# Kernel optimization log

Measured on AMD Instinct MI355X. Metric: run time of the kernel, lower is better.

Reference implementation:

```python
import jax, jax.numpy as jnp
import numpy as np

N_HEADS = 16
N_KV_HEADS = 4
HEAD_DIM = 128


def apply_rope(x, cos, sin):
    # x: [b, h, s, head_dim]; cos/sin: [1, 1, s, head_dim//2]
    d = x.shape[-1] // 2
    x1, x2 = x[..., :d], x[..., d:]
    return jnp.concatenate([x1 * cos - x2 * sin, x1 * sin + x2 * cos], axis=-1)


def setup_inputs() -> dict:
    key = jax.random.key(0)
    ks = jax.random.split(key, 9)
    b, s, dim = 2, 2048, 2048
    inp = {
        "x": jax.random.normal(ks[0], (b, s, dim), jnp.float32),
        "cos": jax.random.normal(ks[1], (1, 1, s, HEAD_DIM // 2), jnp.float32),
        "sin": jax.random.normal(ks[2], (1, 1, s, HEAD_DIM // 2), jnp.float32),
        "Wq": jax.random.normal(ks[3], (dim, N_HEADS * HEAD_DIM), jnp.float32) * 0.02,
        "bq": jax.random.normal(ks[4], (N_HEADS * HEAD_DIM,), jnp.float32) * 0.02,
        "Wkv": jax.random.normal(ks[5], (dim, 2 * N_KV_HEADS * HEAD_DIM), jnp.float32) * 0.02,
        "bkv": jax.random.normal(ks[6], (2 * N_KV_HEADS * HEAD_DIM,), jnp.float32) * 0.02,
        "Wo": jax.random.normal(ks[7], (N_HEADS * HEAD_DIM, dim), jnp.float32) * 0.02,
        "bo": jax.random.normal(ks[8], (dim,), jnp.float32) * 0.02,
        "causal": 1,
    }
    return inp


def reference(x, cos, sin, Wq, bq, Wkv, bkv, Wo, bo, causal):
    b, s, dim = x.shape
    scale = 1.0 / np.sqrt(HEAD_DIM)
    # QKV projections (torch Linear with weight stored transposed here)
    q = (x @ Wq + bq).reshape(b, s, N_HEADS, HEAD_DIM).transpose(0, 2, 1, 3)
    kv = x @ Wkv + bkv  # [b, s, 2*n_kv*hd]
    k, v = jnp.split(kv, 2, axis=-1)
    k = k.reshape(b, s, N_KV_HEADS, HEAD_DIM).transpose(0, 2, 1, 3)
    v = v.reshape(b, s, N_KV_HEADS, HEAD_DIM).transpose(0, 2, 1, 3)
    q = apply_rope(q, cos, sin)
    k = apply_rope(k, cos, sin)
    # GQA: repeat kv heads
    rep = N_HEADS // N_KV_HEADS
    k = jnp.repeat(k, rep, axis=1)
    v = jnp.repeat(v, rep, axis=1)
    logits = jnp.einsum("bhqd,bhkd->bhqk", q, k) * scale
    if causal:
        mask = jnp.tril(jnp.ones((s, s), dtype=bool))
        logits = jnp.where(mask[None, None], logits, jnp.finfo(logits.dtype).min)
    scores = jax.nn.softmax(logits, axis=-1)
    vo = jnp.einsum("bhqk,bhkd->bhqd", scores, v)
    vo = vo.transpose(0, 2, 1, 3).reshape(b, s, N_HEADS * HEAD_DIM)
    out = vo @ Wo + bo
    return out
```

## Files before the change

kernel.cpp:

```cpp
#include <hip/hip_runtime.h>
#include <hip/hip_bf16.h>

typedef __bf16 bf16x8 __attribute__((ext_vector_type(8)));
typedef float  f32x4  __attribute__((ext_vector_type(4)));
typedef unsigned int u32;

#define GLD_LDS16(gp, lp) __builtin_amdgcn_global_load_lds( \
    (const __attribute__((address_space(1))) u32*)(gp), \
    (__attribute__((address_space(3))) u32*)(lp), 16, 0, 0)

template<int CTRL>
__device__ __forceinline__ float dpp_rot(float x) {
    int y = __builtin_amdgcn_update_dpp(__float_as_int(x), __float_as_int(x),
                                        CTRL, 0xF, 0xF, false);
    return __int_as_float(y);
}
__device__ __forceinline__ float rowmax16(float x) {
    x = fmaxf(x, dpp_rot<0x121>(x));
    x = fmaxf(x, dpp_rot<0x122>(x));
    x = fmaxf(x, dpp_rot<0x124>(x));
    x = fmaxf(x, dpp_rot<0x128>(x));
    return x;
}
__device__ __forceinline__ float rowsum16(float x) {
    x += dpp_rot<0x121>(x);
    x += dpp_rot<0x122>(x);
    x += dpp_rot<0x124>(x);
    x += dpp_rot<0x128>(x);
    return x;
}


__global__ __launch_bounds__(256) void f32_to_bf16_kernel(
    const float* __restrict__ in, __bf16* __restrict__ out, size_t n) {
    size_t i = ((size_t)blockIdx.x * 256 + threadIdx.x) * 8;
    if (i >= n) return;
    float4 a = *(const float4*)(in + i);
    float4 b = *(const float4*)(in + i + 4);
    bf16x8 v;
    v[0] = (__bf16)a.x; v[1] = (__bf16)a.y; v[2] = (__bf16)a.z; v[3] = (__bf16)a.w;
    v[4] = (__bf16)b.x; v[5] = (__bf16)b.y; v[6] = (__bf16)b.z; v[7] = (__bf16)b.w;
    *(bf16x8*)(out + i) = v;
}

__global__ __launch_bounds__(256) void transpose_to_bf16_kernel(
    const float* __restrict__ W, __bf16* __restrict__ Wt, int K, int N) {
    __shared__ float tile[32][33];
    int n0 = blockIdx.x * 32, k0 = blockIdx.y * 32;
    int tx = threadIdx.x, ty = threadIdx.y;
    #pragma unroll
    for (int i = 0; i < 32; i += 8)
        tile[ty + i][tx] = W[(size_t)(k0 + ty + i) * N + n0 + tx];
    __syncthreads();
    #pragma unroll
    for (int i = 0; i < 32; i += 8)
        Wt[(size_t)(n0 + ty + i) * K + k0 + tx] = (__bf16)tile[tx][ty + i];
}

__global__ __launch_bounds__(256) void transpose_v_kernel(
    const __bf16* __restrict__ kv, __bf16* __restrict__ vtg, int S) {
    __shared__ __bf16 tile[32][33];
    int s0 = blockIdx.x * 32, d0 = blockIdx.y * 32, z = blockIdx.z;
    int b = z >> 2, kvh = z & 3;
    int tx = threadIdx.x, ty = threadIdx.y;
    #pragma unroll
    for (int i = 0; i < 32; i += 8)
        tile[ty + i][tx] = kv[((size_t)b * S + s0 + ty + i) * 1024 + 512 + kvh * 128 + d0 + tx];
    __syncthreads();
    #pragma unroll
    for (int i = 0; i < 32; i += 8)
        vtg[((size_t)z * 128 + d0 + ty + i) * S + s0 + tx] = tile[tx][ty + i];
}

#define BM 128
#define BN 128
#define BK 32

template <typename OutT>
__global__ __launch_bounds__(256) void gemm_bt_bias_kernel(
    const __bf16* __restrict__ A, const __bf16* __restrict__ Bt,
    const float* __restrict__ bias, OutT* __restrict__ C,
    int M, int N, int K) {
    __shared__ __bf16 As[BM][BK];
    __shared__ __bf16 Bs[BN][BK];
    int tid  = threadIdx.x;
    int bm   = blockIdx.x;
    int bn   = blockIdx.y;
    int wave = tid >> 6;
    int lane = tid & 63;
    int wm   = (wave >> 1) * 64;
    int wn   = (wave & 1) * 64;
    int quad = lane >> 4;
    int l16  = lane & 15;
    int srow = wave * 16 + (lane >> 2);
    int scol = (lane & 3) * 8;

    f32x4 acc[4][4];
    f32x4 zero = {0.f, 0.f, 0.f, 0.f};
    #pragma unroll
    for (int i = 0; i < 4; ++i)
        #pragma unroll
        for (int j = 0; j < 4; ++j) acc[i][j] = zero;

    const __bf16* Abase = A  + (size_t)(bm * BM) * K;
    const __bf16* Bbase = Bt + (size_t)(bn * BN) * K;

    for (int k0 = 0; k0 < K; k0 += BK) {
        if (k0) __syncthreads();
        #pragma unroll
        for (int it = 0; it < 2; ++it) {
            int r = it * 64 + srow;
            GLD_LDS16(Abase + (size_t)r * K + k0 + scol, &As[it * 64 + wave * 16][0]);
            GLD_LDS16(Bbase + (size_t)r * K + k0 + scol, &Bs[it * 64 + wave * 16][0]);
        }
        __syncthreads();

        bf16x8 a_frag[4], b_frag[4];
        #pragma unroll
        for (int i = 0; i < 4; ++i)
            a_frag[i] = *(bf16x8*)(&As[wm + i * 16 + l16][quad * 8]);
        #pragma unroll
        for (int j = 0; j < 4; ++j)
            b_frag[j] = *(bf16x8*)(&Bs[wn + j * 16 + l16][quad * 8]);
        #pragma unroll
        for (int i = 0; i < 4; ++i)
            #pragma unroll
            for (int j = 0; j < 4; ++j)
                acc[i][j] = __builtin_amdgcn_mfma_f32_16x16x32_bf16(
                    a_frag[i], b_frag[j], acc[i][j], 0, 0, 0);
    }

    #pragma unroll
    for (int i = 0; i < 4; ++i) {
        int row = bm * BM + wm + i * 16 + quad * 4;
        #pragma unroll
        for (int j = 0; j < 4; ++j) {
            int col  = bn * BN + wn + j * 16 + l16;
            float bv = bias[col];
            #pragma unroll
            for (int r = 0; r < 4; ++r)
                C[(size_t)(row + r) * N + col] = (OutT)(acc[i][j][r] + bv);
        }
    }
}

__global__ __launch_bounds__(256) void rope_kernel(
    __bf16* __restrict__ buf, const float* __restrict__ cosp,
    const float* __restrict__ sinp, int heads, int rowstride, int S, int total) {
    int idx = blockIdx.x * 256 + threadIdx.x;
    if (idx >= total) return;
    int d  = idx & 63;
    int t2 = idx >> 6;
    int h  = t2 % heads;
    int r  = t2 / heads;
    int s  = r & (S - 1);
    size_t base = (size_t)r * rowstride + h * 128;
    float x1 = (float)buf[base + d];
    float x2 = (float)buf[base + d + 64];
    float c  = cosp[s * 64 + d];
    float sn = sinp[s * 64 + d];
    buf[base + d]      = (__bf16)(x1 * c - x2 * sn);
    buf[base + d + 64] = (__bf16)(x1 * sn + x2 * c);
}

#define FB_K   64
#define PS_STR 72

__global__ __launch_bounds__(256, 2) void flash_mfma_kernel(
    const __bf16* __restrict__ q,
    const __bf16* __restrict__ kv,
    const __bf16* __restrict__ vtg,
    __bf16* __restrict__ vo,
    const int* __restrict__ causal_p, int S) {
    __shared__ __bf16 Ps[4 * 32 * PS_STR];

    int tid  = threadIdx.x;
    int wave = tid >> 6;
    int lane = tid & 63;
    int quad = lane >> 4;
    int l16  = lane & 15;
    int id   = blockIdx.x;
    int xcd  = id & 7;
    int b    = xcd >> 2;
    int kvh  = xcd & 3;
    int rest = id >> 3;
    int qt   = 15 - (rest >> 2);
    int h    = kvh * 4 + (rest & 3);
    int q0   = qt * 128;
    int causal = causal_p[0];
    const float SCALE = 0.08838834764831845f;

    bf16x8 a_frag[2][4];
    #pragma unroll
    for (int mt = 0; mt < 2; ++mt) {
        size_t qbase = ((size_t)b * S + q0 + mt * 64 + wave * 16 + l16) * 2048
                       + h * 128 + quad * 8;
        #pragma unroll
        for (int kc = 0; kc < 4; ++kc)
            a_frag[mt][kc] = *(const bf16x8*)(q + qbase + kc * 32);
    }

    f32x4 o_acc[2][8];
    f32x4 zero4 = {0.f, 0.f, 0.f, 0.f};
    #pragma unroll
    for (int mt = 0; mt < 2; ++mt)
        #pragma unroll
        for (int dt = 0; dt < 8; ++dt) o_acc[mt][dt] = zero4;
    float m_[2][4], l_[2][4];
    #pragma unroll
    for (int mt = 0; mt < 2; ++mt)
        #pragma unroll
        for (int r = 0; r < 4; ++r) { m_[mt][r] = -1e30f; l_[mt][r] = 0.f; }

    const __bf16* kbase = kv  + ((size_t)b * S) * 1024 + kvh * 128;
    const __bf16* vbase = vtg + ((size_t)(b * 4 + kvh) * 128) * S;

    int ntiles = causal ? (2 * qt + 2) : (S / FB_K);
    for (int t = 0; t < ntiles; ++t) {
        int j0 = t * FB_K;

        bf16x8 kf[4][4];
        #pragma unroll
        for (int jt = 0; jt < 4; ++jt) {
            const __bf16* kp = kbase + (size_t)(j0 + jt * 16 + l16) * 1024 + quad * 8;
            #pragma unroll
            for (int kc = 0; kc < 4; ++kc) kf[jt][kc] = *(const bf16x8*)(kp + kc * 32);
        }

        f32x4 s_t[2][4];
        #pragma unroll
        for (int mt = 0; mt < 2; ++mt)
            #pragma unroll
            for (int jt = 0; jt < 4; ++jt) s_t[mt][jt] = zero4;
        #pragma unroll
        for (int jt = 0; jt < 4; ++jt)
            #pragma unroll
            for (int mt = 0; mt < 2; ++mt)
                #pragma unroll
                for (int kc = 0; kc < 4; ++kc)
                    s_t[mt][jt] = __builtin_amdgcn_mfma_f32_16x16x32_bf16(
                        a_frag[mt][kc], kf[jt][kc], s_t[mt][jt], 0, 0, 0);

        bf16x8 vf[8][2];
        #pragma unroll
        for (int dt = 0; dt < 8; ++dt) {
            const __bf16* vp = vbase + (size_t)(dt * 16 + l16) * S + j0 + quad * 8;
            vf[dt][0] = *(const bf16x8*)(vp);
            vf[dt][1] = *(const bf16x8*)(vp + 32);
        }

        int diag = causal && (t >= 2 * qt);
        #pragma unroll
        for (int mt = 0; mt < 2; ++mt) {
            int qrow = q0 + mt * 64 + wave * 16 + quad * 4;
            #pragma unroll
            for (int jt = 0; jt < 4; ++jt)
                #pragma unroll
                for (int r = 0; r < 4; ++r) {
                    float sv = s_t[mt][jt][r] * SCALE;
                    if (diag && (j0 + jt * 16 + l16 > qrow + r)) sv = -1e30f;
                    s_t[mt][jt][r] = sv;
                }
        }

        #pragma unroll
        for (int mt = 0; mt < 2; ++mt) {
            float alpha[4];
            #pragma unroll
            for (int r = 0; r < 4; ++r) {
                float v = fmaxf(fmaxf(s_t[mt][0][r], s_t[mt][1][r]),
                                fmaxf(s_t[mt][2][r], s_t[mt][3][r]));
                v = rowmax16(v);
                float m_new = fmaxf(m_[mt][r], v);
                alpha[r] = __expf(m_[mt][r] - m_new);
                m_[mt][r] = m_new;
                float rs = 0.f;
                #pragma unroll
                for (int jt = 0; jt < 4; ++jt) {
                    float p = __expf(s_t[mt][jt][r] - m_new);
                    s_t[mt][jt][r] = p;
                    rs += p;
                }
                l_[mt][r] = l_[mt][r] * alpha[r] + rs;
            }
            #pragma unroll
            for (int jt = 0; jt < 4; ++jt)
                #pragma unroll
                for (int r = 0; r < 4; ++r)
                    Ps[(wave * 32 + mt * 16 + quad * 4 + r) * PS_STR + jt * 16 + l16] =
                        (__bf16)s_t[mt][jt][r];
            #pragma unroll
            for (int dt = 0; dt < 8; ++dt)
                #pragma unroll
                for (int r = 0; r < 4; ++r) o_acc[mt][dt][r] *= alpha[r];
        }

        bf16x8 p_frag[2][2];
        #pragma unroll
        for (int mt = 0; mt < 2; ++mt) {
            p_frag[mt][0] = *(bf16x8*)&Ps[(wave * 32 + mt * 16 + l16) * PS_STR + quad * 8];
            p_frag[mt][1] = *(bf16x8*)&Ps[(wave * 32 + mt * 16 + l16) * PS_STR + 32 + quad * 8];
        }
        #pragma unroll
        for (int dt = 0; dt < 8; ++dt)
            #pragma unroll
            for (int mt = 0; mt < 2; ++mt) {
                o_acc[mt][dt] = __builtin_amdgcn_mfma_f32_16x16x32_bf16(
                    p_frag[mt][0], vf[dt][0], o_acc[mt][dt], 0, 0, 0);
                o_acc[mt][dt] = __builtin_amdgcn_mfma_f32_16x16x32_bf16(
                    p_frag[mt][1], vf[dt][1], o_acc[mt][dt], 0, 0, 0);
            }
    }

    #pragma unroll
    for (int mt = 0; mt < 2; ++mt) {
        float invl[4];
        #pragma unroll
        for (int r = 0; r < 4; ++r) invl[r] = 1.f / rowsum16(l_[mt][r]);
        size_t obase = ((size_t)b * S + q0 + mt * 64 + wave * 16 + quad * 4) * 2048
                       + h * 128 + l16;
        #pragma unroll
        for (int dt = 0; dt < 8; ++dt)
            #pragma unroll
            for (int r = 0; r < 4; ++r)
                vo[obase + (size_t)r * 2048 + dt * 16] = (__bf16)(o_acc[mt][dt][r] * invl[r]);
    }
}


extern "C" void kernel_launch(void* const* d_in, const int* in_sizes, int n_in,
                              void* d_out, int out_size, void* d_ws, size_t ws_size,
                              hipStream_t stream) {
    const float* x    = (const float*)d_in[0];
    const float* cosp = (const float*)d_in[1];
    const float* sinp = (const float*)d_in[2];
    const float* Wq   = (const float*)d_in[3];
    const float* bq   = (const float*)d_in[4];
    const float* Wkv  = (const float*)d_in[5];
    const float* bkv  = (const float*)d_in[6];
    const float* Wo   = (const float*)d_in[7];
    const float* bo   = (const float*)d_in[8];
    const int* causal = (const int*)d_in[9];
    float* out = (float*)d_out;

    const int B = 2, S = 2048;
    const int M = B * S;

    char* w = (char*)d_ws;
    __bf16* x16   = (__bf16*)w; w += (size_t)M * 2048 * 2;
    __bf16* Wqt   = (__bf16*)w; w += (size_t)2048 * 2048 * 2;
    __bf16* Wkvt  = (__bf16*)w; w += (size_t)1024 * 2048 * 2;
    __bf16* Wot   = (__bf16*)w; w += (size_t)2048 * 2048 * 2;
    __bf16* qbuf  = (__bf16*)w; w += (size_t)M * 2048 * 2;
    __bf16* kvbuf = (__bf16*)w; w += (size_t)M * 1024 * 2;
    __bf16* vobuf = (__bf16*)w; w += (size_t)M * 2048 * 2;
    __bf16* vtg   = Wqt;

    f32_to_bf16_kernel<<<(M * 2048) / (256 * 8), 256, 0, stream>>>(x, x16, (size_t)M * 2048);
    transpose_to_bf16_kernel<<<dim3(2048 / 32, 2048 / 32), dim3(32, 8), 0, stream>>>(Wq, Wqt, 2048, 2048);
    transpose_to_bf16_kernel<<<dim3(1024 / 32, 2048 / 32), dim3(32, 8), 0, stream>>>(Wkv, Wkvt, 2048, 1024);
    transpose_to_bf16_kernel<<<dim3(2048 / 32, 2048 / 32), dim3(32, 8), 0, stream>>>(Wo, Wot, 2048, 2048);
    gemm_bt_bias_kernel<__bf16><<<dim3(M / BM, 2048 / BN), 256, 0, stream>>>(x16, Wqt, bq, qbuf, M, 2048, 2048);
    gemm_bt_bias_kernel<__bf16><<<dim3(M / BM, 1024 / BN), 256, 0, stream>>>(x16, Wkvt, bkv, kvbuf, M, 1024, 2048);
    {
        int totq = M * 16 * 64;
        rope_kernel<<<(totq + 255) / 256, 256, 0, stream>>>(qbuf, cosp, sinp, 16, 2048, S, totq);
        int totk = M * 4 * 64;
        rope_kernel<<<(totk + 255) / 256, 256, 0, stream>>>(kvbuf, cosp, sinp, 4, 1024, S, totk);
    }
    transpose_v_kernel<<<dim3(S / 32, 128 / 32, B * 4), dim3(32, 8), 0, stream>>>(kvbuf, vtg, S);
    flash_mfma_kernel<<<dim3(512), 256, 0, stream>>>(qbuf, kvbuf, vtg, vobuf, causal, S);
    gemm_bt_bias_kernel<float><<<dim3(M / BM, 2048 / BN), 256, 0, stream>>>(vobuf, Wot, bo, out, M, 2048, 2048);
}
```

Before: 463.9 us.

## Fuse QKV GEMM, deepen GEMM K tile, restructure flash attention with LDS K prefetch

Concatenates Wq and Wkv (and their biases) so a single GEMM produces a combined QKV buffer, and raises the GEMM K-tile from 32 to 64 so each barrier pair feeds twice as many MFMAs. The flash kernel now handles 64-row query tiles in two phases, pairing a short and a long causal tile per block for load balance. K tiles are double-buffered into LDS via global_load_lds instead of per-wave global loads. This trades extra LDS use (which may limit occupancy) and more launch-free fusion for fewer launches and better reuse.

```diff
diff --git a/kernel.cpp b/kernel.cpp
--- a/kernel.cpp
+++ b/kernel.cpp
@@ -57,15 +57,24 @@
         Wt[(size_t)(n0 + ty + i) * K + k0 + tx] = (__bf16)tile[tx][ty + i];
 }
 
+__global__ __launch_bounds__(256) void concat_bias_kernel(
+    const float* __restrict__ bq, const float* __restrict__ bkv,
+    float* __restrict__ bqkv) {
+    int i = blockIdx.x * 256 + threadIdx.x;
+    if (i < 2048) bqkv[i] = bq[i];
+    else if (i < 3072) bqkv[i] = bkv[i - 2048];
+}
+
 __global__ __launch_bounds__(256) void transpose_v_kernel(
-    const __bf16* __restrict__ kv, __bf16* __restrict__ vtg, int S) {
+    const __bf16* __restrict__ qkv, __bf16* __restrict__ vtg, int S) {
     __shared__ __bf16 tile[32][33];
     int s0 = blockIdx.x * 32, d0 = blockIdx.y * 32, z = blockIdx.z;
     int b = z >> 2, kvh = z & 3;
     int tx = threadIdx.x, ty = threadIdx.y;
     #pragma unroll
     for (int i = 0; i < 32; i += 8)
-        tile[ty + i][tx] = kv[((size_t)b * S + s0 + ty + i) * 1024 + 512 + kvh * 128 + d0 + tx];
+        tile[ty + i][tx] =
+            qkv[((size_t)b * S + s0 + ty + i) * 3072 + 2560 + kvh * 128 + d0 + tx];
     __syncthreads();
     #pragma unroll
     for (int i = 0; i < 32; i += 8)
@@ -74,15 +83,15 @@
 
 #define BM 128
 #define BN 128
-#define BK 32
+#define BK 64
 
 template <typename OutT>
 __global__ __launch_bounds__(256) void gemm_bt_bias_kernel(
     const __bf16* __restrict__ A, const __bf16* __restrict__ Bt,
     const float* __restrict__ bias, OutT* __restrict__ C,
     int M, int N, int K) {
-    __shared__ __bf16 As[BM][BK];
-    __shared__ __bf16 Bs[BN][BK];
+    __shared__ __bf16 As[BM * BK];
+    __shared__ __bf16 Bs[BN * BK];
     int tid  = threadIdx.x;
     int bm   = blockIdx.x;
     int bn   = blockIdx.y;
@@ -92,8 +101,8 @@
     int wn   = (wave & 1) * 64;
     int quad = lane >> 4;
     int l16  = lane & 15;
-    int srow = wave * 16 + (lane >> 2);
-    int scol = (lane & 3) * 8;
+    int gr   = wave * 32 + (lane >> 3);
+    int gc   = (lane & 7) * 8;
 
     f32x4 acc[4][4];
     f32x4 zero = {0.f, 0.f, 0.f, 0.f};
@@ -108,26 +117,33 @@
     for (int k0 = 0; k0 < K; k0 += BK) {
         if (k0) __syncthreads();
         #pragma unroll
-        for (int it = 0; it < 2; ++it) {
-            int r = it * 64 + srow;
-            GLD_LDS16(Abase + (size_t)r * K + k0 + scol, &As[it * 64 + wave * 16][0]);
-            GLD_LDS16(Bbase + (size_t)r * K + k0 + scol, &Bs[it * 64 + wave * 16][0]);
+        for (int i = 0; i < 4; ++i) {
+            GLD_LDS16(Abase + (size_t)(gr + i * 8) * K + k0 + gc,
+                      &As[(wave * 32 + i * 8) * BK]);
+            GLD_LDS16(Bbase + (size_t)(gr + i * 8) * K + k0 + gc,
+                      &Bs[(wave * 32 + i * 8) * BK]);
         }
         __syncthreads();
 
-        bf16x8 a_frag[4], b_frag[4];
+        bf16x8 af[4][2], bf[4][2];
         #pragma unroll
         for (int i = 0; i < 4; ++i)
-            a_frag[i] = *(bf16x8*)(&As[wm + i * 16 + l16][quad * 8]);
+            #pragma unroll
+            for (int kc = 0; kc < 2; ++kc)
+                af[i][kc] = *(bf16x8*)&As[(wm + i * 16 + l16) * BK + kc * 32 + quad * 8];
         #pragma unroll
         for (int j = 0; j < 4; ++j)
-            b_frag[j] = *(bf16x8*)(&Bs[wn + j * 16 + l16][quad * 8]);
-        #pragma unroll
-        for (int i = 0; i < 4; ++i)
-            #pragma unroll
-            for (int j = 0; j < 4; ++j)
-                acc[i][j] = __builtin_amdgcn_mfma_f32_16x16x32_bf16(
-                    a_frag[i], b_frag[j], acc[i][j], 0, 0, 0);
+            #pragma unroll
+            for (int kc = 0; kc < 2; ++kc)
+                bf[j][kc] = *(bf16x8*)&Bs[(wn + j * 16 + l16) * BK + kc * 32 + quad * 8];
+        #pragma unroll
+        for (int kc = 0; kc < 2; ++kc)
+            #pragma unroll
+            for (int i = 0; i < 4; ++i)
+                #pragma unroll
+                for (int j = 0; j < 4; ++j)
+                    acc[i][j] = __builtin_amdgcn_mfma_f32_16x16x32_bf16(
+                        af[i][kc], bf[j][kc], acc[i][j], 0, 0, 0);
     }
 
     #pragma unroll
@@ -146,7 +162,8 @@
 
 __global__ __launch_bounds__(256) void rope_kernel(
     __bf16* __restrict__ buf, const float* __restrict__ cosp,
-    const float* __restrict__ sinp, int heads, int rowstride, int S, int total) {
+    const float* __restrict__ sinp, int heads, int rowstride, int coloff,
+    int S, int total) {
     int idx = blockIdx.x * 256 + threadIdx.x;
     if (idx >= total) return;
     int d  = idx & 63;
@@ -154,7 +171,7 @@
     int h  = t2 % heads;
     int r  = t2 / heads;
     int s  = r & (S - 1);
-    size_t base = (size_t)r * rowstride + h * 128;
+    size_t base = (size_t)r * rowstride + coloff + h * 128;
     float x1 = (float)buf[base + d];
     float x2 = (float)buf[base + d + 64];
     float c  = cosp[s * 64 + d];
@@ -163,17 +180,17 @@
     buf[base + d + 64] = (__bf16)(x1 * sn + x2 * c);
 }
 
-#define FB_K   64
 #define PS_STR 72
 
 __global__ __launch_bounds__(256, 2) void flash_mfma_kernel(
-    const __bf16* __restrict__ q,
-    const __bf16* __restrict__ kv,
+    const __bf16* __restrict__ qkv,
     const __bf16* __restrict__ vtg,
     __bf16* __restrict__ vo,
     const int* __restrict__ causal_p, int S) {
-    __shared__ __bf16 Ps[4 * 32 * PS_STR];
-
+    __shared__ __bf16 Ks[2][64 * 128];
+    __shared__ __bf16 Ps[4 * 16 * PS_STR];
+
+    const int QKV = 3072;
     int tid  = threadIdx.x;
     int wave = tid >> 6;
     int lane = tid & 63;
@@ -184,146 +201,135 @@
     int b    = xcd >> 2;
     int kvh  = xcd & 3;
     int rest = id >> 3;
-    int qt   = 15 - (rest >> 2);
-    int h    = kvh * 4 + (rest & 3);
-    int q0   = qt * 128;
+    int hh   = rest & 3;
+    int pair = rest >> 2;
+    int h    = kvh * 4 + hh;
     int causal = causal_p[0];
     const float SCALE = 0.08838834764831845f;
 
-    bf16x8 a_frag[2][4];
-    #pragma unroll
-    for (int mt = 0; mt < 2; ++mt) {
-        size_t qbase = ((size_t)b * S + q0 + mt * 64 + wave * 16 + l16) * 2048
-                       + h * 128 + quad * 8;
+    const __bf16* vB = vtg + ((size_t)(b * 4 + kvh) * 128) * S;
+
+    #pragma unroll 1
+    for (int phase = 0; phase < 2; ++phase) {
+        int qt = phase ? (31 - pair) : pair;
+        int q0 = qt * 64;
+        int nt = causal ? (qt + 1) : (S / 64);
+
+        bf16x8 a_frag[4];
+        size_t qrow = ((size_t)b * S + q0 + wave * 16 + l16) * QKV + h * 128 + quad * 8;
         #pragma unroll
         for (int kc = 0; kc < 4; ++kc)
-            a_frag[mt][kc] = *(const bf16x8*)(q + qbase + kc * 32);
-    }
-
-    f32x4 o_acc[2][8];
-    f32x4 zero4 = {0.f, 0.f, 0.f, 0.f};
-    #pragma unroll
-    for (int mt = 0; mt < 2; ++mt)
-        #pragma unroll
-        for (int dt = 0; dt < 8; ++dt) o_acc[mt][dt] = zero4;
-    float m_[2][4], l_[2][4];
-    #pragma unroll
-    for (int mt = 0; mt < 2; ++mt)
-        #pragma unroll
-        for (int r = 0; r < 4; ++r) { m_[mt][r] = -1e30f; l_[mt][r] = 0.f; }
-
-    const __bf16* kbase = kv  + ((size_t)b * S) * 1024 + kvh * 128;
-    const __bf16* vbase = vtg + ((size_t)(b * 4 + kvh) * 128) * S;
-
-    int ntiles = causal ? (2 * qt + 2) : (S / FB_K);
-    for (int t = 0; t < ntiles; ++t) {
-        int j0 = t * FB_K;
-
-        bf16x8 kf[4][4];
-        #pragma unroll
-        for (int jt = 0; jt < 4; ++jt) {
-            const __bf16* kp = kbase + (size_t)(j0 + jt * 16 + l16) * 1024 + quad * 8;
-            #pragma unroll
-            for (int kc = 0; kc < 4; ++kc) kf[jt][kc] = *(const bf16x8*)(kp + kc * 32);
+            a_frag[kc] = *(const bf16x8*)(qkv + qrow + kc * 32);
+
+        f32x4 o_acc[8];
+        f32x4 zero4 = {0.f, 0.f, 0.f, 0.f};
+        #pragma unroll
+        for (int dt = 0; dt < 8; ++dt) o_acc[dt] = zero4;
+        float m_[4], l_[4];
+        #pragma unroll
+        for (int r = 0; r < 4; ++r) { m_[r] = -1e30f; l_[r] = 0.f; }
+        int qrow_d = q0 + wave * 16 + quad * 4;
+
+        __syncthreads();
+        {
+            size_t kg = ((size_t)b * S + wave * 16 + l16) * QKV + 2048 + kvh * 128 + quad * 8;
+            #pragma unroll
+            for (int kc = 0; kc < 4; ++kc)
+                GLD_LDS16(qkv + kg + kc * 32, &Ks[0][(wave * 4 + kc) * 512]);
         }
 
-        f32x4 s_t[2][4];
-        #pragma unroll
-        for (int mt = 0; mt < 2; ++mt)
-            #pragma unroll
-            for (int jt = 0; jt < 4; ++jt) s_t[mt][jt] = zero4;
-        #pragma unroll
-        for (int jt = 0; jt < 4; ++jt)
-            #pragma unroll
-            for (int mt = 0; mt < 2; ++mt)
+        for (int t = 0; t < nt; ++t) {
+            int cur = t & 1;
+            __syncthreads();
+            if (t + 1 < nt) {
+                size_t kg = ((size_t)b * S + (t + 1) * 64 + wave * 16 + l16) * QKV
+                            + 2048 + kvh * 128 + quad * 8;
                 #pragma unroll
                 for (int kc = 0; kc < 4; ++kc)
-                    s_t[mt][jt] = __builtin_amdgcn_mfma_f32_16x16x32_bf16(
-                        a_frag[mt][kc], kf[jt][kc], s_t[mt][jt], 0, 0, 0);
-
-        bf16x8 vf[8][2];
-        #pragma unroll
-        for (int dt = 0; dt < 8; ++dt) {
-            const __bf16* vp = vbase + (size_t)(dt * 16 + l16) * S + j0 + quad * 8;
-            vf[dt][0] = *(const bf16x8*)(vp);
-            vf[dt][1] = *(const bf16x8*)(vp + 32);
-        }
-
-        int diag = causal && (t >= 2 * qt);
-        #pragma unroll
-        for (int mt = 0; mt < 2; ++mt) {
-            int qrow = q0 + mt * 64 + wave * 16 + quad * 4;
+                    GLD_LDS16(qkv + kg + kc * 32, &Ks[1 - cur][(wave * 4 + kc) * 512]);
+            }
+            int j0 = t * 64;
+
+            bf16x8 vf[8][2];
+            #pragma unroll
+            for (int dt = 0; dt < 8; ++dt) {
+                const __bf16* vp = vB + (size_t)(dt * 16 + l16) * S + j0 + quad * 8;
+                vf[dt][0] = *(const bf16x8*)(vp);
+                vf[dt][1] = *(const bf16x8*)(vp + 32);
+            }
+
+            f32x4 s_t[4];
+            #pragma unroll
+            for (int jt = 0; jt < 4; ++jt) s_t[jt] = zero4;
             #pragma unroll
             for (int jt = 0; jt < 4; ++jt)
                 #pragma unroll
+                for (int kc = 0; kc < 4; ++kc) {
+                    bf16x8 kf = *(bf16x8*)&Ks[cur][(jt * 4 + kc) * 512 + lane * 8];
+                    s_t[jt] = __builtin_amdgcn_mfma_f32_16x16x32_bf16(
+                        a_frag[kc], kf, s_t[jt], 0, 0, 0);
+                }
+
+            int diag = causal && (t == nt - 1);
+            #pragma unroll
+            for (int jt = 0; jt < 4; ++jt)
+                #pragma unroll
                 for (int r = 0; r < 4; ++r) {
-                    float sv = s_t[mt][jt][r] * SCALE;
-                    if (diag && (j0 + jt * 16 + l16 > qrow + r)) sv = -1e30f;
-                    s_t[mt][jt][r] = sv;
+                    float sv = s_t[jt][r] * SCALE;
+                    if (diag && (j0 + jt * 16 + l16 > qrow_d + r)) sv = -1e30f;
+                    s_t[jt][r] = sv;
                 }
-        }
-
-        #pragma unroll
-        for (int mt = 0; mt < 2; ++mt) {
+
             float alpha[4];
             #pragma unroll
             for (int r = 0; r < 4; ++r) {
-                float v = fmaxf(fmaxf(s_t[mt][0][r], s_t[mt][1][r]),
-                                fmaxf(s_t[mt][2][r], s_t[mt][3][r]));
+                float v = fmaxf(fmaxf(s_t[0][r], s_t[1][r]),
+                                fmaxf(s_t[2][r], s_t[3][r]));
                 v = rowmax16(v);
-                float m_new = fmaxf(m_[mt][r], v);
-                alpha[r] = __expf(m_[mt][r] - m_new);
-                m_[mt][r] = m_new;
+                float m_new = fmaxf(m_[r], v);
+                alpha[r] = __expf(m_[r] - m_new);
+                m_[r] = m_new;
                 float rs = 0.f;
                 #pragma unroll
                 for (int jt = 0; jt < 4; ++jt) {
-                    float p = __expf(s_t[mt][jt][r] - m_new);
-                    s_t[mt][jt][r] = p;
+                    float p = __expf(s_t[jt][r] - m_new);
+                    s_t[jt][r] = p;
                     rs += p;
                 }
-                l_[mt][r] = l_[mt][r] * alpha[r] + rs;
+                l_[r] = l_[r] * alpha[r] + rs;
             }
             #pragma unroll
             for (int jt = 0; jt < 4; ++jt)
                 #pragma unroll
                 for (int r = 0; r < 4; ++r)
-                    Ps[(wave * 32 + mt * 16 + quad * 4 + r) * PS_STR + jt * 16 + l16] =
-                        (__bf16)s_t[mt][jt][r];
+                    Ps[(wave * 16 + quad * 4 + r) * PS_STR + jt * 16 + l16] =
+                        (__bf16)s_t[jt][r];
             #pragma unroll
             for (int dt = 0; dt < 8; ++dt)
                 #pragma unroll
-                for (int r = 0; r < 4; ++r) o_acc[mt][dt][r] *= alpha[r];
+                for (int r = 0; r < 4; ++r) o_acc[dt][r] *= alpha[r];
+
+            bf16x8 p0 = *(bf16x8*)&Ps[(wave * 16 + l16) * PS_STR + quad * 8];
+            bf16x8 p1 = *(bf16x8*)&Ps[(wave * 16 + l16) * PS_STR + 32 + quad * 8];
+            #pragma unroll
+            for (int dt = 0; dt < 8; ++dt) {
+                o_acc[dt] = __builtin_amdgcn_mfma_f32_16x16x32_bf16(
+                    p0, vf[dt][0], o_acc[dt], 0, 0, 0);
+                o_acc[dt] = __builtin_amdgcn_mfma_f32_16x16x32_bf16(
+                    p1, vf[dt][1], o_acc[dt], 0, 0, 0);
+            }
         }
 
-        bf16x8 p_frag[2][2];
-        #pragma unroll
-        for (int mt = 0; mt < 2; ++mt) {
-            p_frag[mt][0] = *(bf16x8*)&Ps[(wave * 32 + mt * 16 + l16) * PS_STR + quad * 8];
-            p_frag[mt][1] = *(bf16x8*)&Ps[(wave * 32 + mt * 16 + l16) * PS_STR + 32 + quad * 8];
-        }
+        float invl[4];
+        #pragma unroll
+        for (int r = 0; r < 4; ++r) invl[r] = 1.f / rowsum16(l_[r]);
+        size_t obase = ((size_t)b * S + q0 + wave * 16 + quad * 4) * 2048
+                       + h * 128 + l16;
         #pragma unroll
         for (int dt = 0; dt < 8; ++dt)
             #pragma unroll
-            for (int mt = 0; mt < 2; ++mt) {
-                o_acc[mt][dt] = __builtin_amdgcn_mfma_f32_16x16x32_bf16(
-                    p_frag[mt][0], vf[dt][0], o_acc[mt][dt], 0, 0, 0);
-                o_acc[mt][dt] = __builtin_amdgcn_mfma_f32_16x16x32_bf16(
-                    p_frag[mt][1], vf[dt][1], o_acc[mt][dt], 0, 0, 0);
-            }
-    }
-
-    #pragma unroll
-    for (int mt = 0; mt < 2; ++mt) {
-        float invl[4];
-        #pragma unroll
-        for (int r = 0; r < 4; ++r) invl[r] = 1.f / rowsum16(l_[mt][r]);
-        size_t obase = ((size_t)b * S + q0 + mt * 64 + wave * 16 + quad * 4) * 2048
-                       + h * 128 + l16;
-        #pragma unroll
-        for (int dt = 0; dt < 8; ++dt)
-            #pragma unroll
             for (int r = 0; r < 4; ++r)
-                vo[obase + (size_t)r * 2048 + dt * 16] = (__bf16)(o_acc[mt][dt][r] * invl[r]);
+                vo[obase + (size_t)r * 2048 + dt * 16] = (__bf16)(o_acc[dt][r] * invl[r]);
     }
 }
 
@@ -347,28 +353,27 @@
     const int M = B * S;
 
     char* w = (char*)d_ws;
-    __bf16* x16   = (__bf16*)w; w += (size_t)M * 2048 * 2;
-    __bf16* Wqt   = (__bf16*)w; w += (size_t)2048 * 2048 * 2;
-    __bf16* Wkvt  = (__bf16*)w; w += (size_t)1024 * 2048 * 2;
-    __bf16* Wot   = (__bf16*)w; w += (size_t)2048 * 2048 * 2;
-    __bf16* qbuf  = (__bf16*)w; w += (size_t)M * 2048 * 2;
-    __bf16* kvbuf = (__bf16*)w; w += (size_t)M * 1024 * 2;
-    __bf16* vobuf = (__bf16*)w; w += (size_t)M * 2048 * 2;
-    __bf16* vtg   = Wqt;
+    __bf16* x16    = (__bf16*)w; w += (size_t)M * 2048 * 2;
+    __bf16* Wqkvt  = (__bf16*)w; w += (size_t)3072 * 2048 * 2;
+    __bf16* Wot    = (__bf16*)w; w += (size_t)2048 * 2048 * 2;
+    float*  bqkv   = (float*)w;  w += (size_t)3072 * 4;
+    __bf16* qkvbuf = (__bf16*)w; w += (size_t)M * 3072 * 2;
+    __bf16* vobuf  = x16;
+    __bf16* vtg    = Wqkvt;
 
     f32_to_bf16_kernel<<<(M * 2048) / (256 * 8), 256, 0, stream>>>(x, x16, (size_t)M * 2048);
-    transpose_to_bf16_kernel<<<dim3(2048 / 32, 2048 / 32), dim3(32, 8), 0, stream>>>(Wq, Wqt, 2048, 2048);
-    transpose_to_bf16_kernel<<<dim3(1024 / 32, 2048 / 32), dim3(32, 8), 0, stream>>>(Wkv, Wkvt, 2048, 1024);
+    transpose_to_bf16_kernel<<<dim3(2048 / 32, 2048 / 32), dim3(32, 8), 0, stream>>>(Wq, Wqkvt, 2048, 2048);
+    transpose_to_bf16_kernel<<<dim3(1024 / 32, 2048 / 32), dim3(32, 8), 0, stream>>>(Wkv, Wqkvt + (size_t)2048 * 2048, 2048, 1024);
     transpose_to_bf16_kernel<<<dim3(2048 / 32, 2048 / 32), dim3(32, 8), 0, stream>>>(Wo, Wot, 2048, 2048);
-    gemm_bt_bias_kernel<__bf16><<<dim3(M / BM, 2048 / BN), 256, 0, stream>>>(x16, Wqt, bq, qbuf, M, 2048, 2048);
-    gemm_bt_bias_kernel<__bf16><<<dim3(M / BM, 1024 / BN), 256, 0, stream>>>(x16, Wkvt, bkv, kvbuf, M, 1024, 2048);
+    concat_bias_kernel<<<12, 256, 0, stream>>>(bq, bkv, bqkv);
+    gemm_bt_bias_kernel<__bf16><<<dim3(M / BM, 3072 / BN), 256, 0, stream>>>(x16, Wqkvt, bqkv, qkvbuf, M, 3072, 2048);
     {
         int totq = M * 16 * 64;
-        rope_kernel<<<(totq + 255) / 256, 256, 0, stream>>>(qbuf, cosp, sinp, 16, 2048, S, totq);
+        rope_kernel<<<(totq + 255) / 256, 256, 0, stream>>>(qkvbuf, cosp, sinp, 16, 3072, 0, S, totq);
         int totk = M * 4 * 64;
-        rope_kernel<<<(totk + 255) / 256, 256, 0, stream>>>(kvbuf, cosp, sinp, 4, 1024, S, totk);
+        rope_kernel<<<(totk + 255) / 256, 256, 0, stream>>>(qkvbuf, cosp, sinp, 4, 3072, 2048, S, totk);
     }
-    transpose_v_kernel<<<dim3(S / 32, 128 / 32, B * 4), dim3(32, 8), 0, stream>>>(kvbuf, vtg, S);
-    flash_mfma_kernel<<<dim3(512), 256, 0, stream>>>(qbuf, kvbuf, vtg, vobuf, causal, S);
+    transpose_v_kernel<<<dim3(S / 32, 128 / 32, B * 4), dim3(32, 8), 0, stream>>>(qkvbuf, vtg, S);
+    flash_mfma_kernel<<<dim3(512), 256, 0, stream>>>(qkvbuf, vtg, vobuf, causal, S);
     gemm_bt_bias_kernel<float><<<dim3(M / BM, 2048 / BN), 256, 0, stream>>>(vobuf, Wot, bo, out, M, 2048, 2048);
 }
```

New measurement: 431.5 us. -7.0%, faster.
